# Kernel tuning notes

Measured on AMD Instinct MI355X. Metric: run time of the kernel, lower is better.

The kernel has to match this reference:

```python
import jax, jax.numpy as jnp
import numpy as np

EPSILON = 1e-06

def setup_inputs() -> dict:
    key = jax.random.key(0)
    k1, k2, k3 = jax.random.split(key, 3)
    B, S, D = 4, 4096, 4096
    x = jax.random.normal(k1, (B, S, D), dtype=jnp.float32)
    residual = jax.random.normal(k2, (B, S, D), dtype=jnp.float32)
    gamma = jax.random.uniform(k3, (D,), dtype=jnp.float32)
    return {"x": x, "residual": residual, "gamma": gamma}

def reference(x, residual, gamma):
    # Pass 1: residual add + RMSNorm (row-wise over last dim)
    x_added = x + residual
    rstd = jax.lax.rsqrt(jnp.mean(jnp.square(x_added), axis=-1, keepdims=True) + EPSILON)
    output = x_added * rstd * gamma  # [B, S, D]
    # Pass 2: global abs-max dynamic int8 quantization
    max_val = jnp.max(jnp.abs(output))
    scale = max_val / 127.0
    q = jnp.clip(jnp.round(output / scale), -128, 127).astype(jnp.int8)
    return q
```

## Files before the change

kernel.cpp:

```cpp
#include <hip/hip_runtime.h>

#define DD 4096
#define NROWS 16384
#define EPS 1e-6f

typedef float fx4 __attribute__((ext_vector_type(4)));
typedef int   ix4 __attribute__((ext_vector_type(4)));


__global__ __launch_bounds__(256) void pass1(
    const float* __restrict__ x, const float* __restrict__ res,
    const float* __restrict__ gamma, unsigned int* __restrict__ q8,
    float* __restrict__ rowmax) {
  const int row = blockIdx.x;
  const int t = threadIdx.x;
  const fx4* x4 = (const fx4*)(x + (size_t)row * DD);
  const fx4* r4 = (const fx4*)(res + (size_t)row * DD);
  const fx4* g4 = (const fx4*)gamma;

  float ss = 0.f, mx = 0.f;
#pragma unroll
  for (int i = 0; i < 4; ++i) {
    const int idx = t + i * 256;
    fx4 xv = x4[idx], rv = r4[idx], gv = g4[idx];
    fx4 y = xv + rv;
    ss += y.x * y.x + y.y * y.y + y.z * y.z + y.w * y.w;
    fx4 p = y * gv;
    mx = fmaxf(mx, fmaxf(fmaxf(fabsf(p.x), fabsf(p.y)),
                         fmaxf(fabsf(p.z), fabsf(p.w))));
  }
#pragma unroll
  for (int off = 32; off > 0; off >>= 1) {
    ss += __shfl_down(ss, off, 64);
    mx = fmaxf(mx, __shfl_down(mx, off, 64));
  }
  __shared__ float s_ss[4], s_mx[4];
  const int wave = t >> 6, lane = t & 63;
  if (lane == 0) { s_ss[wave] = ss; s_mx[wave] = mx; }
  __syncthreads();
  const float tss = s_ss[0] + s_ss[1] + s_ss[2] + s_ss[3];
  const float tmx = fmaxf(fmaxf(s_mx[0], s_mx[1]), fmaxf(s_mx[2], s_mx[3]));
  const float rs = rsqrtf(tss * (1.0f / DD) + EPS);
  if (t == 0) rowmax[row] = tmx * rs;
  const float inv = tmx > 0.f ? 127.0f / tmx : 0.f;

  unsigned int* qrow = q8 + (size_t)row * (DD / 4);
#pragma unroll
  for (int i = 0; i < 4; ++i) {
    const int idx = t + i * 256;
    fx4 xv = x4[idx], rv = r4[idx], gv = g4[idx];
    fx4 p = (xv + rv) * gv;
    int a = min(max(__float2int_rn(p.x * inv), -127), 127);
    int b = min(max(__float2int_rn(p.y * inv), -127), 127);
    int c = min(max(__float2int_rn(p.z * inv), -127), 127);
    int d = min(max(__float2int_rn(p.w * inv), -127), 127);
    qrow[idx] = (unsigned int)(a & 255) | ((unsigned int)(b & 255) << 8) |
                ((unsigned int)(c & 255) << 16) | ((unsigned int)(d & 255) << 24);
  }
}

__global__ __launch_bounds__(1024) void reduce_gmax(
    const float* __restrict__ rowmax, float* __restrict__ gmax) {
  const int t = threadIdx.x;
  float m = 0.f;
#pragma unroll
  for (int i = 0; i < NROWS / 1024; ++i) m = fmaxf(m, rowmax[t + i * 1024]);
#pragma unroll
  for (int off = 32; off > 0; off >>= 1) m = fmaxf(m, __shfl_down(m, off, 64));
  __shared__ float s[16];
  if ((t & 63) == 0) s[t >> 6] = m;
  __syncthreads();
  if (t == 0) {
    float r = s[0];
#pragma unroll
    for (int i = 1; i < 16; ++i) r = fmaxf(r, s[i]);
    *gmax = r;
  }
}

__global__ __launch_bounds__(256) void pass2(
    const unsigned int* __restrict__ q8, const float* __restrict__ rowmax,
    const float* __restrict__ gmax, int* __restrict__ out) {
  const int row = blockIdx.x;
  const float c = rowmax[row] / *gmax;
  const unsigned int* qrow = q8 + (size_t)row * (DD / 4);
  ix4* orow = (ix4*)(out + (size_t)row * DD);
#pragma unroll
  for (int i = 0; i < 4; ++i) {
    const int idx = threadIdx.x + i * 256;
    const unsigned int w = qrow[idx];
    ix4 q;
    q.x = min(max(__float2int_rn((float)((int)(w << 24) >> 24) * c), -128), 127);
    q.y = min(max(__float2int_rn((float)((int)(w << 16) >> 24) * c), -128), 127);
    q.z = min(max(__float2int_rn((float)((int)(w << 8) >> 24) * c), -128), 127);
    q.w = min(max(__float2int_rn((float)((int)w >> 24) * c), -128), 127);
    orow[idx] = q;
  }
}

__global__ __launch_bounds__(256) void pass1_nb(
    const float* __restrict__ x, const float* __restrict__ res,
    const float* __restrict__ gamma, float* __restrict__ rstd,
    float* __restrict__ rowmax) {
  const int row = blockIdx.x;
  const int t = threadIdx.x;
  const fx4* x4 = (const fx4*)(x + (size_t)row * DD);
  const fx4* r4 = (const fx4*)(res + (size_t)row * DD);
  const fx4* g4 = (const fx4*)gamma;
  float ss = 0.f, mx = 0.f;
#pragma unroll
  for (int i = 0; i < 4; ++i) {
    const int idx = t + i * 256;
    fx4 xv = x4[idx], rv = r4[idx], gv = g4[idx];
    fx4 y = xv + rv;
    ss += y.x * y.x + y.y * y.y + y.z * y.z + y.w * y.w;
    fx4 p = y * gv;
    mx = fmaxf(mx, fmaxf(fmaxf(fabsf(p.x), fabsf(p.y)),
                         fmaxf(fabsf(p.z), fabsf(p.w))));
  }
#pragma unroll
  for (int off = 32; off > 0; off >>= 1) {
    ss += __shfl_down(ss, off, 64);
    mx = fmaxf(mx, __shfl_down(mx, off, 64));
  }
  __shared__ float s_ss[4], s_mx[4];
  const int wave = t >> 6, lane = t & 63;
  if (lane == 0) { s_ss[wave] = ss; s_mx[wave] = mx; }
  __syncthreads();
  if (t == 0) {
    float tss = s_ss[0] + s_ss[1] + s_ss[2] + s_ss[3];
    float tmx = fmaxf(fmaxf(s_mx[0], s_mx[1]), fmaxf(s_mx[2], s_mx[3]));
    float rs = rsqrtf(tss * (1.0f / DD) + EPS);
    rstd[row] = rs;
    rowmax[row] = tmx * rs;
  }
}

__global__ __launch_bounds__(256) void pass2_nb(
    const float* __restrict__ x, const float* __restrict__ res,
    const float* __restrict__ gamma, const float* __restrict__ rstd,
    const float* __restrict__ gmax, int* __restrict__ out) {
  const int row = blockIdx.x;
  const int t = threadIdx.x;
  const float c = rstd[row] * (127.0f / *gmax);
  const fx4* x4 = (const fx4*)(x + (size_t)row * DD);
  const fx4* r4 = (const fx4*)(res + (size_t)row * DD);
  const fx4* g4 = (const fx4*)gamma;
  ix4* o4 = (ix4*)(out + (size_t)row * DD);
#pragma unroll
  for (int i = 0; i < 4; ++i) {
    const int idx = t + i * 256;
    fx4 xv = x4[idx], rv = r4[idx], gv = g4[idx];
    ix4 q;
    q.x = min(max(__float2int_rn((xv.x + rv.x) * gv.x * c), -128), 127);
    q.y = min(max(__float2int_rn((xv.y + rv.y) * gv.y * c), -128), 127);
    q.z = min(max(__float2int_rn((xv.z + rv.z) * gv.z * c), -128), 127);
    q.w = min(max(__float2int_rn((xv.w + rv.w) * gv.w * c), -128), 127);
    o4[idx] = q;
  }
}

extern "C" void kernel_launch(void* const* d_in, const int* in_sizes, int n_in,
                              void* d_out, int out_size, void* d_ws, size_t ws_size,
                              hipStream_t stream) {
  const float* x     = (const float*)d_in[0];
  const float* res   = (const float*)d_in[1];
  const float* gamma = (const float*)d_in[2];
  int* out = (int*)d_out;

  char* ws = (char*)d_ws;
  float* gmax   = (float*)ws;
  float* rowmax = (float*)(ws + 256);
  float* rstd   = (float*)(ws + 256 + 64 * 1024);
  const size_t q8_off = (size_t)1 << 20;
  const size_t need = q8_off + (size_t)NROWS * DD;

  if (ws_size >= need) {
    unsigned int* q8 = (unsigned int*)(ws + q8_off);
    pass1<<<NROWS, 256, 0, stream>>>(x, res, gamma, q8, rowmax);
    reduce_gmax<<<1, 1024, 0, stream>>>(rowmax, gmax);
    pass2<<<NROWS, 256, 0, stream>>>(q8, rowmax, gmax, out);
  } else {
    pass1_nb<<<NROWS, 256, 0, stream>>>(x, res, gamma, rstd, rowmax);
    reduce_gmax<<<1, 1024, 0, stream>>>(rowmax, gmax);
    pass2_nb<<<NROWS, 256, 0, stream>>>(x, res, gamma, rstd, gmax, out);
  }
}
```

Measured before the change: 196.4 us.

## Keep normalized values in registers and stage packed int8 inside output buffer

pass1 now keeps the gamma-scaled values in registers across the block reduction, so it no longer reloads x, residual and gamma for the quantization step. It then writes each thread's sixteen packed int8 values as one 16-byte store into the start of that row's slot in the output buffer, instead of into a separate workspace area. pass2 reads the packed data back from the same row and expands it to the final int32 values in place. This removes the second read of the inputs and the separate workspace buffer, and may help cache locality because the staging bytes sit in the lines that will later be overwritten. The cost is higher register pressure in pass1 and an in-place read-then-write pattern whose correctness relies on each thread reading its own slot before any thread of the block overwrites it.

```diff
diff --git a/kernel.cpp b/kernel.cpp
--- a/kernel.cpp
+++ b/kernel.cpp
@@ -10,7 +10,7 @@
 
 __global__ __launch_bounds__(256) void pass1(
     const float* __restrict__ x, const float* __restrict__ res,
-    const float* __restrict__ gamma, unsigned int* __restrict__ q8,
+    const float* __restrict__ gamma, unsigned int* __restrict__ outw,
     float* __restrict__ rowmax) {
   const int row = blockIdx.x;
   const int t = threadIdx.x;
@@ -18,16 +18,16 @@
   const fx4* r4 = (const fx4*)(res + (size_t)row * DD);
   const fx4* g4 = (const fx4*)gamma;
 
+  fx4 p[4];
   float ss = 0.f, mx = 0.f;
 #pragma unroll
   for (int i = 0; i < 4; ++i) {
     const int idx = t + i * 256;
-    fx4 xv = x4[idx], rv = r4[idx], gv = g4[idx];
-    fx4 y = xv + rv;
+    fx4 y = x4[idx] + r4[idx];
     ss += y.x * y.x + y.y * y.y + y.z * y.z + y.w * y.w;
-    fx4 p = y * gv;
-    mx = fmaxf(mx, fmaxf(fmaxf(fabsf(p.x), fabsf(p.y)),
-                         fmaxf(fabsf(p.z), fabsf(p.w))));
+    p[i] = y * g4[idx];
+    mx = fmaxf(mx, fmaxf(fmaxf(fabsf(p[i].x), fabsf(p[i].y)),
+                         fmaxf(fabsf(p[i].z), fabsf(p[i].w))));
   }
 #pragma unroll
   for (int off = 32; off > 0; off >>= 1) {
@@ -44,19 +44,17 @@
   if (t == 0) rowmax[row] = tmx * rs;
   const float inv = tmx > 0.f ? 127.0f / tmx : 0.f;
 
-  unsigned int* qrow = q8 + (size_t)row * (DD / 4);
+  ix4 d;
+  int* dp = (int*)&d;
 #pragma unroll
   for (int i = 0; i < 4; ++i) {
-    const int idx = t + i * 256;
-    fx4 xv = x4[idx], rv = r4[idx], gv = g4[idx];
-    fx4 p = (xv + rv) * gv;
-    int a = min(max(__float2int_rn(p.x * inv), -127), 127);
-    int b = min(max(__float2int_rn(p.y * inv), -127), 127);
-    int c = min(max(__float2int_rn(p.z * inv), -127), 127);
-    int d = min(max(__float2int_rn(p.w * inv), -127), 127);
-    qrow[idx] = (unsigned int)(a & 255) | ((unsigned int)(b & 255) << 8) |
-                ((unsigned int)(c & 255) << 16) | ((unsigned int)(d & 255) << 24);
+    int a = min(max(__float2int_rn(p[i].x * inv), -127), 127);
+    int b = min(max(__float2int_rn(p[i].y * inv), -127), 127);
+    int c = min(max(__float2int_rn(p[i].z * inv), -127), 127);
+    int e = min(max(__float2int_rn(p[i].w * inv), -127), 127);
+    dp[i] = (a & 255) | ((b & 255) << 8) | ((c & 255) << 16) | ((e & 255) << 24);
   }
+  *(ix4*)(outw + (size_t)row * DD + 4 * t) = d;
 }
 
 __global__ __launch_bounds__(1024) void reduce_gmax(
@@ -79,22 +77,23 @@
 }
 
 __global__ __launch_bounds__(256) void pass2(
-    const unsigned int* __restrict__ q8, const float* __restrict__ rowmax,
+    unsigned int* __restrict__ outw, const float* __restrict__ rowmax,
     const float* __restrict__ gmax, int* __restrict__ out) {
   const int row = blockIdx.x;
+  const int t = threadIdx.x;
   const float c = rowmax[row] / *gmax;
-  const unsigned int* qrow = q8 + (size_t)row * (DD / 4);
+  union { ix4 v; unsigned int w[4]; } u;
+  u.v = *(const ix4*)(outw + (size_t)row * DD + 4 * t);
   ix4* orow = (ix4*)(out + (size_t)row * DD);
 #pragma unroll
   for (int i = 0; i < 4; ++i) {
-    const int idx = threadIdx.x + i * 256;
-    const unsigned int w = qrow[idx];
+    const unsigned int w = u.w[i];
     ix4 q;
     q.x = min(max(__float2int_rn((float)((int)(w << 24) >> 24) * c), -128), 127);
     q.y = min(max(__float2int_rn((float)((int)(w << 16) >> 24) * c), -128), 127);
     q.z = min(max(__float2int_rn((float)((int)(w << 8) >> 24) * c), -128), 127);
     q.w = min(max(__float2int_rn((float)((int)w >> 24) * c), -128), 127);
-    orow[idx] = q;
+    orow[t + i * 256] = q;
   }
 }
 
@@ -111,10 +110,9 @@
 #pragma unroll
   for (int i = 0; i < 4; ++i) {
     const int idx = t + i * 256;
-    fx4 xv = x4[idx], rv = r4[idx], gv = g4[idx];
-    fx4 y = xv + rv;
+    fx4 y = x4[idx] + r4[idx];
     ss += y.x * y.x + y.y * y.y + y.z * y.z + y.w * y.w;
-    fx4 p = y * gv;
+    fx4 p = y * g4[idx];
     mx = fmaxf(mx, fmaxf(fmaxf(fabsf(p.x), fabsf(p.y)),
                          fmaxf(fabsf(p.z), fabsf(p.w))));
   }
@@ -172,14 +170,12 @@
   float* gmax   = (float*)ws;
   float* rowmax = (float*)(ws + 256);
   float* rstd   = (float*)(ws + 256 + 64 * 1024);
-  const size_t q8_off = (size_t)1 << 20;
-  const size_t need = q8_off + (size_t)NROWS * DD;
 
-  if (ws_size >= need) {
-    unsigned int* q8 = (unsigned int*)(ws + q8_off);
-    pass1<<<NROWS, 256, 0, stream>>>(x, res, gamma, q8, rowmax);
+  if (ws_size >= (size_t)(2 << 20)) {
+    unsigned int* outw = (unsigned int*)d_out;
+    pass1<<<NROWS, 256, 0, stream>>>(x, res, gamma, outw, rowmax);
     reduce_gmax<<<1, 1024, 0, stream>>>(rowmax, gmax);
-    pass2<<<NROWS, 256, 0, stream>>>(q8, rowmax, gmax, out);
+    pass2<<<NROWS, 256, 0, stream>>>(outw, rowmax, gmax, out);
   } else {
     pass1_nb<<<NROWS, 256, 0, stream>>>(x, res, gamma, rstd, rowmax);
     reduce_gmax<<<1, 1024, 0, stream>>>(rowmax, gmax);
```

Measured after the change: 191.4 us. -2.6%, faster.
